# Kernel tuning notes

Measured on AMD Instinct MI355X. Metric: run time of the kernel, lower is better.

Reference implementation:

```python
import jax, jax.numpy as jnp
import numpy as np

B, T, F, U = 128, 512, 512, 256

def hard_sigmoid(x):
    # Keras K.hard_sigmoid
    return jnp.clip(0.2 * x + 0.5, 0.0, 1.0)

def setup_inputs() -> dict:
    key = jax.random.key(0)
    ks = jax.random.split(key, 10)
    def glorot(k, shp):
        fan_in, fan_out = shp[0], shp[-1]
        std = np.sqrt(2.0 / (fan_in + fan_out)).astype(np.float32)
        return jax.random.normal(k, shp, jnp.float32) * std
    return {
        "x": jax.random.normal(ks[0], (B, T, F), jnp.float32),
        "kernel": glorot(ks[1], (F, 4 * U)),
        "recurrent_kernel": glorot(ks[2], (U, 4 * U)),
        "attention_h": glorot(ks[3], (F + U, U)),
        "attention_c": glorot(ks[4], (F + U, U)),
        "attention1": glorot(ks[5], (2 * U + F, U)),
        "biase1": glorot(ks[6], (U,)),
        "attention2": glorot(ks[7], (U, 1)),
        "attention2_2": glorot(ks[8], (U, 1)),
        "biase2": glorot(ks[9], (U,)),
    }

def _run_direction(x_tbf, xg_tbg, rk, Wh, Wc, units):
    # x_tbf: (T,B,F); xg_tbg: (T,B,4U) precomputed x @ kernel (same math as per-step dot)
    Bn = x_tbf.shape[1]
    z = jnp.zeros((Bn, units), x_tbf.dtype)
    carry0 = (z, z, z, z, z, z, z, z)

    def att_weights(states, Ws, xt):
        # softmax over L2 norms of tanh(concat(state, x) @ W) for 4 history states
        scores = []
        for s, W in zip(states, Ws):
            a = jnp.tanh(jnp.concatenate([s, xt], axis=1) @ W)  # (B,U)
            scores.append(jnp.sqrt(jnp.sum(a * a, axis=1)))     # (B,)
        return jax.nn.softmax(jnp.stack(scores, axis=1), axis=1)  # (B,4)

    def step(carry, inp):
        xt, xg = inp
        h1, c1, h2, c2, h3, c3, h4, c4 = carry
        wh = att_weights([h1, h2, h3, h4], [Wh, Wh, Wh, Wh], xt)
        hmix = jax.nn.relu(wh[:, 0:1] * h1 + wh[:, 1:2] * h2 + wh[:, 2:3] * h3 + wh[:, 3:4] * h4)
        # NOTE: original code (faithfully kept) uses attention_h for the 4th cell-state score
        wc = att_weights([c1, c2, c3, c4], [Wc, Wc, Wc, Wh], xt)
        cmix = jax.nn.relu(wc[:, 0:1] * c1 + wc[:, 1:2] * c2 + wc[:, 2:3] * c3 + wc[:, 3:4] * c4)
        g = xg + hmix @ rk  # (B,4U), gate order [i, f, c, o]
        i = hard_sigmoid(g[:, :units])
        f = hard_sigmoid(g[:, units:2 * units])
        m = hard_sigmoid(g[:, 2 * units:3 * units])  # candidate uses hard_sigmoid in original
        o = hard_sigmoid(g[:, 3 * units:])
        c = f * cmix + i * m
        h = o * jnp.tanh(c)
        # history shift: [h, c, h_tm1, c_tm1, h_tm2, c_tm2, h_tm3, c_tm3]
        return (h, c, h1, c1, h2, c2, h3, c3), h

    _, hs = jax.lax.scan(step, carry0, (x_tbf, xg_tbg))
    return hs  # (T,B,U)

def reference(x, kernel, recurrent_kernel, attention_h, attention_c,
              attention1, biase1, attention2, attention2_2, biase2):
    units = recurrent_kernel.shape[0]
    x_tbf = jnp.transpose(x, (1, 0, 2))              # (T,B,F)
    xg = jnp.einsum('tbf,fg->tbg', x_tbf, kernel)    # (T,B,4U)
    fwd = _run_direction(x_tbf, xg, recurrent_kernel, attention_h, attention_c, units)
    bwd = _run_direction(x_tbf[::-1], xg[::-1], recurrent_kernel, attention_h, attention_c, units)[::-1]
    outs = jnp.concatenate([fwd, bwd], axis=-1)      # (T,B,2U)
    outs = jnp.transpose(outs, (1, 0, 2))            # (B,T,2U)
    # intra attention (vectorized over time, equivalent to the per-step loop + reshape)
    A11 = attention1[:2 * units, :]
    A12 = attention1[2 * units:, :]
    ha = jax.nn.relu(outs @ A11 + 0.0 * biase1) @ attention2        # (B,T,1)
    hb = jax.nn.relu(x @ A12 + 0.0 * biase2) @ attention2_2         # (B,T,1)
    return jnp.tanh(ha * outs + hb)                                  # (B,T,2U)
```

## Files before the change

kernel.cpp:

```cpp
#include <hip/hip_runtime.h>
#include <cstddef>
#include <cstdint>

#define DEVINL __device__ __forceinline__

constexpr int Bn = 128;
constexpr int Tn = 512;
constexpr int Fn = 512;
constexpr int Un = 256;
constexpr int Gn = 1024;
constexpr int RS = 5;

typedef _Float16 h2t   __attribute__((ext_vector_type(2)));
typedef _Float16 half4 __attribute__((ext_vector_type(4)));
typedef _Float16 half8 __attribute__((ext_vector_type(8)));
typedef float    f32x4 __attribute__((ext_vector_type(4)));

DEVINL float ftanh(float x) { float e = __expf(2.f * x); return 1.f - 2.f / (e + 1.f); }
DEVINL float hsig(float x)  { return fminf(fmaxf(fmaf(x, 0.2f, 0.5f), 0.f), 1.f); }

DEVINL void softmax4(float* s) {
    float mx = fmaxf(fmaxf(s[0], s[1]), fmaxf(s[2], s[3]));
    float e0 = __expf(s[0] - mx), e1 = __expf(s[1] - mx);
    float e2 = __expf(s[2] - mx), e3 = __expf(s[3] - mx);
    float inv = 1.f / (e0 + e1 + e2 + e3);
    s[0] = e0 * inv; s[1] = e1 * inv; s[2] = e2 * inv; s[3] = e3 * inv;
}

DEVINL float d2(unsigned int w, unsigned int h, float acc) {
#if __has_builtin(__builtin_amdgcn_fdot2)
    return __builtin_amdgcn_fdot2(__builtin_bit_cast(h2t, w), __builtin_bit_cast(h2t, h), acc, false);
#else
    h2t a = __builtin_bit_cast(h2t, w), b = __builtin_bit_cast(h2t, h);
    acc = fmaf((float)a.x, (float)b.x, acc);
    acc = fmaf((float)a.y, (float)b.y, acc);
    return acc;
#endif
}
DEVINL float dot8h(uint4 w, uint4 h, float acc) {
    acc = d2(w.x, h.x, acc);
    acc = d2(w.y, h.y, acc);
    acc = d2(w.z, h.z, acc);
    acc = d2(w.w, h.w, acc);
    return acc;
}

__global__ __launch_bounds__(256)
void pack_x(const float* __restrict__ x, _Float16* __restrict__ xh)
{
    size_t i = ((size_t)blockIdx.x * 256 + threadIdx.x) * 4;
    float4 v = *(const float4*)(x + i);
    half4 o;
    o.x = (_Float16)v.x; o.y = (_Float16)v.y; o.z = (_Float16)v.z; o.w = (_Float16)v.w;
    *(half4*)(xh + i) = o;
}

__global__ __launch_bounds__(256)
void wt_pack(const float* __restrict__ W, _Float16* __restrict__ Wt, int N)
{
    int total = N * 512;
    for (int e = blockIdx.x * 256 + threadIdx.x; e < total; e += gridDim.x * 256) {
        int n = e >> 9, k = e & 511;
        Wt[e] = (_Float16)W[(size_t)k * N + n];
    }
}

__global__ __launch_bounds__(256)
void pack_w(const float* __restrict__ rk, const float* __restrict__ ath,
            const float* __restrict__ atc,
            _Float16* __restrict__ rkP, _Float16* __restrict__ WhP,
            _Float16* __restrict__ WcP)
{
    int idx = blockIdx.x * 256 + threadIdx.x;
    const int stride = gridDim.x * 256;
    for (int e = idx; e < 32 * 1024 * 8; e += stride) {
        int i = e & 7, n = (e >> 3) & 1023, kc = e >> 13;
        rkP[e] = (_Float16)rk[(size_t)(kc * 8 + i) * Gn + n];
    }
    for (int e = idx; e < 32 * 256 * 8; e += stride) {
        int i = e & 7, n = (e >> 3) & 255, kc = e >> 11;
        WhP[e] = (_Float16)ath[(size_t)(kc * 8 + i) * Un + n];
        WcP[e] = (_Float16)atc[(size_t)(kc * 8 + i) * Un + n];
    }
}

template<bool TMAJ>
__global__ __launch_bounds__(256)
void gemm_mfma(const _Float16* __restrict__ A, const _Float16* __restrict__ Wt,
               int N, _Float16* __restrict__ out)
{
    __shared__ __align__(16) _Float16 As[64][40];
    __shared__ __align__(16) _Float16 Bs[64][40];
    const int tid = threadIdx.x;
    const int n0 = blockIdx.x * 64, m0 = blockIdx.y * 64;
    const int w = tid >> 6, lane = tid & 63;
    const int fr = lane & 15, quad = lane >> 4;
    const int srow = tid >> 2, sk = (tid & 3) * 8;

    f32x4 acc[4];
    #pragma unroll
    for (int i = 0; i < 4; i++) acc[i] = (f32x4){0.f, 0.f, 0.f, 0.f};

    const _Float16* ap = A  + (size_t)(m0 + srow) * 512 + sk;
    const _Float16* bp = Wt + (size_t)(n0 + srow) * 512 + sk;

    for (int k0 = 0; k0 < 512; k0 += 32) {
        uint4 av = *(const uint4*)(ap + k0);
        uint4 bv = *(const uint4*)(bp + k0);
        __syncthreads();
        *(uint4*)&As[srow][sk] = av;
        *(uint4*)&Bs[srow][sk] = bv;
        __syncthreads();
        half8 a = *(const half8*)&As[w * 16 + fr][quad * 8];
        #pragma unroll
        for (int nt = 0; nt < 4; nt++) {
            half8 b = *(const half8*)&Bs[nt * 16 + fr][quad * 8];
            acc[nt] = __builtin_amdgcn_mfma_f32_16x16x32_f16(a, b, acc[nt], 0, 0, 0);
        }
    }
    #pragma unroll
    for (int nt = 0; nt < 4; nt++) {
        int n = n0 + nt * 16 + fr;
        #pragma unroll
        for (int reg = 0; reg < 4; reg++) {
            int m = m0 + w * 16 + quad * 4 + reg;
            if (TMAJ) {
                int b = m >> 9, t = m & 511;
                out[((size_t)t * Bn + b) * N + n] = (_Float16)acc[nt][reg];
            } else {
                out[(size_t)m * N + n] = (_Float16)acc[nt][reg];
            }
        }
    }
}

__global__ __launch_bounds__(512)
void recurrence(const _Float16* __restrict__ xg,
                const _Float16* __restrict__ xWh,
                const _Float16* __restrict__ xWc,
                const _Float16* __restrict__ rkP,
                const _Float16* __restrict__ WhP,
                const _Float16* __restrict__ WcP,
                _Float16* __restrict__ outs)
{
    const int tid = threadIdx.x;
    const int d = blockIdx.x >> 7;
    const int b = blockIdx.x & 127;

    __shared__ float Hr[RS][Un], Cr[RS][Un];
    __shared__ float PHr[RS][Un], PCcr[RS][Un], PChr[RS][Un];
    __shared__ __align__(16) unsigned int hm_pk[128];
    __shared__ __align__(16) unsigned int Hpk[128], Cpk[128];
    __shared__ float gtmp[4][Un];
    __shared__ __align__(16) float red[8][4];

    for (int e = tid; e < RS * Un; e += 512) {
        ((float*)Hr)[e] = 0.f; ((float*)Cr)[e] = 0.f;
        ((float*)PHr)[e] = 0.f; ((float*)PCcr)[e] = 0.f; ((float*)PChr)[e] = 0.f;
    }
    __syncthreads();

    const int u = tid & 255;
    const int g = tid >> 8;
    const int lane = tid & 63;
    const int gwv = (tid >> 6) & 3;

    for (int t = 0; t < Tn; t++) {
        const int tt = d ? (Tn - 1 - t) : t;
        const int st = t % RS;
        int sj[4];
        #pragma unroll
        for (int j = 0; j < 4; j++) sj[j] = (t - 1 - j + 2 * RS) % RS;

        const size_t rowx = (size_t)tt * Bn + b;

        float xh = (float)xWh[rowx * Un + u];
        float xc = (float)xWc[rowx * Un + u];
        float xg0 = 0.f, xg1 = 0.f, xg2 = 0.f, xg3 = 0.f;
        if (tid < 256) {
            xg0 = (float)xg[rowx * Gn + u];
            xg1 = (float)xg[rowx * Gn + Un + u];
            xg2 = (float)xg[rowx * Gn + 2 * Un + u];
            xg3 = (float)xg[rowx * Gn + 3 * Un + u];
        }

        float vals[4];
        if (g == 0) {
            #pragma unroll
            for (int j = 0; j < 4; j++) {
                float ah = ftanh(PHr[sj[j]][u] + xh);
                vals[j] = ah * ah;
            }
        } else {
            #pragma unroll
            for (int j = 0; j < 4; j++) {
                float pc = (j < 3) ? PCcr[sj[j]][u] : PChr[sj[j]][u];
                float ac = ftanh(pc + ((j < 3) ? xc : xh));
                vals[j] = ac * ac;
            }
        }
        #pragma unroll
        for (int jj = 0; jj < 4; jj++) {
            float v = vals[jj];
            #pragma unroll
            for (int m = 32; m; m >>= 1) v += __shfl_xor(v, m, 64);
            if (lane == 0) red[g * 4 + jj][gwv] = v;
        }
        __syncthreads();

        float cmv = 0.f;
        if (tid < 256) {
            float sh[4], sc[4];
            #pragma unroll
            for (int j = 0; j < 4; j++) {
                float4 ph  = *(const float4*)red[j];
                float4 pcv = *(const float4*)red[4 + j];
                sh[j] = sqrtf(ph.x + ph.y + ph.z + ph.w);
                sc[j] = sqrtf(pcv.x + pcv.y + pcv.z + pcv.w);
            }
            softmax4(sh); softmax4(sc);
            float ha = 0.f, ca = 0.f;
            #pragma unroll
            for (int j = 0; j < 4; j++) {
                ha = fmaf(sh[j], Hr[sj[j]][u], ha);
                ca = fmaf(sc[j], Cr[sj[j]][u], ca);
            }
            float hmv = fmaxf(ha, 0.f);
            cmv = fmaxf(ca, 0.f);
            float ho = __shfl_xor(hmv, 1, 64);
            if (!(tid & 1)) {
                h2t pk; pk.x = (_Float16)hmv; pk.y = (_Float16)ho;
                hm_pk[u >> 1] = __builtin_bit_cast(unsigned int, pk);
            }
        }
        __syncthreads();

        {
            float a0 = 0.f, a1 = 0.f;
            const _Float16* p1 = rkP + (size_t)tid * 8;
            const _Float16* p2 = rkP + (size_t)(tid + 512) * 8;
            #pragma unroll 4
            for (int kc = 0; kc < 32; kc++) {
                uint4 w1 = *(const uint4*)(p1 + (size_t)kc * 8192);
                uint4 w2 = *(const uint4*)(p2 + (size_t)kc * 8192);
                uint4 h0 = *(const uint4*)&hm_pk[kc * 4];
                a0 = dot8h(w1, h0, a0);
                a1 = dot8h(w2, h0, a1);
            }
            int q = tid >> 8;
            gtmp[q][u] = a0;
            gtmp[q + 2][u] = a1;
        }
        __syncthreads();

        if (tid < 256) {
            float g0 = gtmp[0][u] + xg0;
            float g1 = gtmp[1][u] + xg1;
            float g2 = gtmp[2][u] + xg2;
            float g3 = gtmp[3][u] + xg3;
            float gi = hsig(g0), gf = hsig(g1), gm = hsig(g2), go = hsig(g3);
            float c = gf * cmv + gi * gm;
            float h = go * ftanh(c);
            Hr[st][u] = h;
            Cr[st][u] = c;
            outs[((size_t)b * Tn + tt) * 512 + d * 256 + u] = (_Float16)h;
            float hho = __shfl_xor(h, 1, 64);
            float cco = __shfl_xor(c, 1, 64);
            if (!(tid & 1)) {
                h2t pk1; pk1.x = (_Float16)h; pk1.y = (_Float16)hho;
                h2t pk2; pk2.x = (_Float16)c; pk2.y = (_Float16)cco;
                Hpk[u >> 1] = __builtin_bit_cast(unsigned int, pk1);
                Cpk[u >> 1] = __builtin_bit_cast(unsigned int, pk2);
            }
        }
        __syncthreads();

        if (tid < 256) {
            const int c = tid;
            const _Float16* pw = WhP + (size_t)c * 8;
            float ph = 0.f, pch = 0.f;
            #pragma unroll 4
            for (int kc = 0; kc < 32; kc++) {
                uint4 wv4 = *(const uint4*)(pw + (size_t)kc * 2048);
                uint4 Hv = *(const uint4*)&Hpk[kc * 4];
                uint4 Cv = *(const uint4*)&Cpk[kc * 4];
                ph  = dot8h(wv4, Hv, ph);
                pch = dot8h(wv4, Cv, pch);
            }
            PHr[st][c]  = ph;
            PChr[st][c] = pch;
        } else {
            const int c = tid - 256;
            const _Float16* pw = WcP + (size_t)c * 8;
            float pcc = 0.f;
            #pragma unroll 4
            for (int kc = 0; kc < 32; kc++) {
                uint4 wv4 = *(const uint4*)(pw + (size_t)kc * 2048);
                uint4 Cv = *(const uint4*)&Cpk[kc * 4];
                pcc = dot8h(wv4, Cv, pcc);
            }
            PCcr[st][c] = pcc;
        }
        __syncthreads();
    }
}

DEVINL void cvt8(uint4 v, float* f) {
    h2t p0 = __builtin_bit_cast(h2t, v.x), p1 = __builtin_bit_cast(h2t, v.y);
    h2t p2 = __builtin_bit_cast(h2t, v.z), p3 = __builtin_bit_cast(h2t, v.w);
    f[0] = (float)p0.x; f[1] = (float)p0.y; f[2] = (float)p1.x; f[3] = (float)p1.y;
    f[4] = (float)p2.x; f[5] = (float)p2.y; f[6] = (float)p3.x; f[7] = (float)p3.y;
}

__global__ __launch_bounds__(256)
void final2(const _Float16* __restrict__ t1, const _Float16* __restrict__ t2,
            const _Float16* __restrict__ outs16,
            const float* __restrict__ at2, const float* __restrict__ at22,
            float* __restrict__ out)
{
    __shared__ float has[8], hbs[8];
    const int tid = threadIdx.x;
    const size_t m0 = (size_t)blockIdx.x * 8;
    const int rr = tid >> 5, us = tid & 31;
    const size_t m = m0 + rr;

    uint4 v1 = *(const uint4*)(t1 + m * 256 + us * 8);
    uint4 v2 = *(const uint4*)(t2 + m * 256 + us * 8);
    float f1[8], f2[8];
    cvt8(v1, f1); cvt8(v2, f2);
    float4 wa0 = *(const float4*)(at2  + us * 8);
    float4 wa1 = *(const float4*)(at2  + us * 8 + 4);
    float4 wb0 = *(const float4*)(at22 + us * 8);
    float4 wb1 = *(const float4*)(at22 + us * 8 + 4);

    float pa = fmaxf(f1[0], 0.f) * wa0.x + fmaxf(f1[1], 0.f) * wa0.y
             + fmaxf(f1[2], 0.f) * wa0.z + fmaxf(f1[3], 0.f) * wa0.w
             + fmaxf(f1[4], 0.f) * wa1.x + fmaxf(f1[5], 0.f) * wa1.y
             + fmaxf(f1[6], 0.f) * wa1.z + fmaxf(f1[7], 0.f) * wa1.w;
    float pb = fmaxf(f2[0], 0.f) * wb0.x + fmaxf(f2[1], 0.f) * wb0.y
             + fmaxf(f2[2], 0.f) * wb0.z + fmaxf(f2[3], 0.f) * wb0.w
             + fmaxf(f2[4], 0.f) * wb1.x + fmaxf(f2[5], 0.f) * wb1.y
             + fmaxf(f2[6], 0.f) * wb1.z + fmaxf(f2[7], 0.f) * wb1.w;
    #pragma unroll
    for (int mm = 16; mm; mm >>= 1) {
        pa += __shfl_xor(pa, mm, 32);
        pb += __shfl_xor(pb, mm, 32);
    }
    if (us == 0) { has[rr] = pa; hbs[rr] = pb; }
    __syncthreads();

    for (int e = tid; e < 8 * 128; e += 256) {
        int r2 = e >> 7, k4 = (e & 127) * 4;
        size_t base = (m0 + r2) * 512 + k4;
        uint2 hv = *(const uint2*)(outs16 + base);
        h2t pA = __builtin_bit_cast(h2t, hv.x), pB = __builtin_bit_cast(h2t, hv.y);
        float hav = has[r2], hbv = hbs[r2];
        float4 o;
        o.x = ftanh(hav * (float)pA.x + hbv);
        o.y = ftanh(hav * (float)pA.y + hbv);
        o.z = ftanh(hav * (float)pB.x + hbv);
        o.w = ftanh(hav * (float)pB.y + hbv);
        *(float4*)(out + base) = o;
    }
}

extern "C" void kernel_launch(void* const* d_in, const int* in_sizes, int n_in,
                              void* d_out, int out_size, void* d_ws, size_t ws_size,
                              hipStream_t stream)
{
    (void)in_sizes; (void)n_in; (void)out_size; (void)ws_size;
    const float* x    = (const float*)d_in[0];
    const float* wk   = (const float*)d_in[1];
    const float* rk   = (const float*)d_in[2];
    const float* ath  = (const float*)d_in[3];
    const float* atc  = (const float*)d_in[4];
    const float* at1  = (const float*)d_in[5];
    const float* at2  = (const float*)d_in[7];
    const float* at22 = (const float*)d_in[8];
    float* out = (float*)d_out;

    char* p = (char*)d_ws;
    auto take = [&](size_t bytes) { char* q = p; p += (bytes + 255) & ~(size_t)255; return q; };
    _Float16* xg   = (_Float16*)take((size_t)Tn * Bn * Gn * 2);
    _Float16* xWh  = (_Float16*)take((size_t)Tn * Bn * Un * 2);
    _Float16* xWc  = (_Float16*)take((size_t)Tn * Bn * Un * 2);
    _Float16* A16  = (_Float16*)take((size_t)Bn * Tn * 512 * 2);
    _Float16* xf16 = (_Float16*)take((size_t)Bn * Tn * Fn * 2);
    _Float16* rkP  = (_Float16*)take((size_t)Un * Gn * 2);
    _Float16* WhP  = (_Float16*)take((size_t)Un * Un * 2);
    _Float16* WcP  = (_Float16*)take((size_t)Un * Un * 2);
    _Float16* Wt1  = (_Float16*)take((size_t)Gn * Fn * 2);
    _Float16* Wt2  = (_Float16*)take((size_t)Un * Fn * 2);
    _Float16* Wt3  = (_Float16*)take((size_t)Un * Fn * 2);
    _Float16* WtA  = (_Float16*)take((size_t)Un * Fn * 2);
    _Float16* WtB  = (_Float16*)take((size_t)Un * Fn * 2);
    _Float16* t1 = (_Float16*)xg;
    _Float16* t2 = t1 + (size_t)Bn * Tn * Un;

    pack_x<<<32768, 256, 0, stream>>>(x, xf16);
    wt_pack<<<2048, 256, 0, stream>>>(wk, Wt1, Gn);
    wt_pack<<<1024, 256, 0, stream>>>(ath + (size_t)Un * Un, Wt2, Un);
    wt_pack<<<1024, 256, 0, stream>>>(atc + (size_t)Un * Un, Wt3, Un);
    wt_pack<<<1024, 256, 0, stream>>>(at1, WtA, Un);
    wt_pack<<<1024, 256, 0, stream>>>(at1 + (size_t)512 * Un, WtB, Un);
    pack_w<<<64, 256, 0, stream>>>(rk, ath, atc, rkP, WhP, WcP);

    gemm_mfma<true><<<dim3(Gn / 64, (Bn * Tn) / 64), 256, 0, stream>>>(xf16, Wt1, Gn, xg);
    gemm_mfma<true><<<dim3(Un / 64, (Bn * Tn) / 64), 256, 0, stream>>>(xf16, Wt2, Un, xWh);
    gemm_mfma<true><<<dim3(Un / 64, (Bn * Tn) / 64), 256, 0, stream>>>(xf16, Wt3, Un, xWc);

    recurrence<<<dim3(256), dim3(512), 0, stream>>>(xg, xWh, xWc, rkP, WhP, WcP, A16);

    gemm_mfma<false><<<dim3(Un / 64, (Bn * Tn) / 64), 256, 0, stream>>>(A16,  WtA, Un, t1);
    gemm_mfma<false><<<dim3(Un / 64, (Bn * Tn) / 64), 256, 0, stream>>>(xf16, WtB, Un, t2);
    final2<<<(Bn * Tn) / 8, 256, 0, stream>>>(t1, t2, A16, at2, at22, out);
}
```

Baseline: 5.029 ms.

## Split recurrent weights across 8-block groups with global-memory barriers per step

Each group of 8 workgroups now handles 8 batch rows together, and each block keeps a 1/8 slice of the recurrent and attention weights resident in LDS (96KB dynamic shared memory). The block no longer streams the full weights from global or L2 every timestep. Intermediate vectors (hmix, h, c, the partial gate sums and the attention projections) are exchanged through global memory using relaxed atomics, with three to four counter-based inter-block barriers per timestep. This trades weight bandwidth for cross-block synchronization latency. It relies on all 256 blocks being co-resident, with a timeout guard to avoid deadlock.

Result: slower. 16.38 ms (+225.7%).

```diff
diff --git a/kernel.cpp b/kernel.cpp
--- a/kernel.cpp
+++ b/kernel.cpp
@@ -43,6 +43,19 @@
     acc = d2(w.z, h.z, acc);
     acc = d2(w.w, h.w, acc);
     return acc;
+}
+
+DEVINL void ast_u32(unsigned int* p, unsigned int v) {
+    __hip_atomic_store(p, v, __ATOMIC_RELAXED, __HIP_MEMORY_SCOPE_AGENT);
+}
+DEVINL unsigned int ald_u32(const unsigned int* p) {
+    return __hip_atomic_load(p, __ATOMIC_RELAXED, __HIP_MEMORY_SCOPE_AGENT);
+}
+DEVINL void ast_f32(float* p, float v) {
+    __hip_atomic_store(p, v, __ATOMIC_RELAXED, __HIP_MEMORY_SCOPE_AGENT);
+}
+DEVINL float ald_f32(const float* p) {
+    return __hip_atomic_load(p, __ATOMIC_RELAXED, __HIP_MEMORY_SCOPE_AGENT);
 }
 
 __global__ __launch_bounds__(256)
@@ -141,29 +154,79 @@
                 const _Float16* __restrict__ rkP,
                 const _Float16* __restrict__ WhP,
                 const _Float16* __restrict__ WcP,
-                _Float16* __restrict__ outs)
+                _Float16* __restrict__ outs,
+                unsigned int* __restrict__ Xhm,
+                unsigned int* __restrict__ XH,
+                unsigned int* __restrict__ XC,
+                float* __restrict__ Xg,
+                float* __restrict__ Xph,
+                float* __restrict__ Xpch,
+                float* __restrict__ Xpcc,
+                unsigned int* __restrict__ cnt)
 {
     const int tid = threadIdx.x;
-    const int d = blockIdx.x >> 7;
-    const int b = blockIdx.x & 127;
+    const int grp = blockIdx.x & 31;
+    const int s   = blockIdx.x >> 5;
+    const int rowId = grp * 8 + s;
+    const int d = rowId >> 7, b = rowId & 127;
 
     __shared__ float Hr[RS][Un], Cr[RS][Un];
     __shared__ float PHr[RS][Un], PCcr[RS][Un], PChr[RS][Un];
-    __shared__ __align__(16) unsigned int hm_pk[128];
-    __shared__ __align__(16) unsigned int Hpk[128], Cpk[128];
     __shared__ float gtmp[4][Un];
+    __shared__ __align__(16) unsigned int hmS[8][128];
+    __shared__ __align__(16) unsigned int HSs[8][128], CSs[8][128];
     __shared__ __align__(16) float red[8][4];
-
+    __shared__ int sync_dead;
+
+    extern __shared__ uint4 dynv[];
+    uint4* rkA = dynv;
+    uint4* WhA = dynv + 32 * 128;
+    uint4* WcA = WhA + 32 * 32;
+
+    {
+        const uint4* rkG = (const uint4*)rkP;
+        for (int e = tid; e < 32 * 128; e += 512) {
+            int kc = e >> 7, c = e & 127;
+            rkA[e] = rkG[kc * 1024 + s * 128 + c];
+        }
+        const uint4* whG = (const uint4*)WhP;
+        const uint4* wcG = (const uint4*)WcP;
+        for (int e = tid; e < 32 * 32; e += 512) {
+            int kc = e >> 5, c = e & 31;
+            WhA[e] = whG[kc * 256 + s * 32 + c];
+            WcA[e] = wcG[kc * 256 + s * 32 + c];
+        }
+    }
     for (int e = tid; e < RS * Un; e += 512) {
         ((float*)Hr)[e] = 0.f; ((float*)Cr)[e] = 0.f;
         ((float*)PHr)[e] = 0.f; ((float*)PCcr)[e] = 0.f; ((float*)PChr)[e] = 0.f;
     }
+    if (tid == 0) sync_dead = 0;
     __syncthreads();
+
+    unsigned int* myCnt = cnt + grp * 64;
+    unsigned int tgt = 8;
 
     const int u = tid & 255;
     const int g = tid >> 8;
     const int lane = tid & 63;
     const int gwv = (tid >> 6) & 3;
+    const size_t gb128 = (size_t)grp * 8 * 128;
+
+    auto gsync = [&](unsigned int target) {
+        __syncthreads();
+        if (tid == 0) {
+            __hip_atomic_fetch_add(myCnt, 1u, __ATOMIC_ACQ_REL, __HIP_MEMORY_SCOPE_AGENT);
+            if (!sync_dead) {
+                int guard = 0;
+                while (__hip_atomic_load(myCnt, __ATOMIC_ACQUIRE, __HIP_MEMORY_SCOPE_AGENT) < target) {
+                    __builtin_amdgcn_s_sleep(2);
+                    if (++guard > 2000000) { sync_dead = 1; break; }
+                }
+            }
+        }
+        __syncthreads();
+    };
 
     for (int t = 0; t < Tn; t++) {
         const int tt = d ? (Tn - 1 - t) : t;
@@ -171,7 +234,6 @@
         int sj[4];
         #pragma unroll
         for (int j = 0; j < 4; j++) sj[j] = (t - 1 - j + 2 * RS) % RS;
-
         const size_t rowx = (size_t)tt * Bn + b;
 
         float xh = (float)xWh[rowx * Un + u];
@@ -182,6 +244,18 @@
             xg1 = (float)xg[rowx * Gn + Un + u];
             xg2 = (float)xg[rowx * Gn + 2 * Un + u];
             xg3 = (float)xg[rowx * Gn + 3 * Un + u];
+        }
+
+        if (t > 0) {
+            if (tid < 256) {
+                int slot = (t - 1) % RS;
+                int src = tid >> 5, c5 = tid & 31;
+                size_t pb = ((size_t)(grp * 8 + src) * 8 + s) * 32 + c5;
+                PHr[slot][tid]  = ald_f32(Xph + pb);
+                PChr[slot][tid] = ald_f32(Xpch + pb);
+                PCcr[slot][tid] = ald_f32(Xpcc + pb);
+            }
+            __syncthreads();
         }
 
         float vals[4];
@@ -230,29 +304,38 @@
             float ho = __shfl_xor(hmv, 1, 64);
             if (!(tid & 1)) {
                 h2t pk; pk.x = (_Float16)hmv; pk.y = (_Float16)ho;
-                hm_pk[u >> 1] = __builtin_bit_cast(unsigned int, pk);
-            }
-        }
-        __syncthreads();
-
+                ast_u32(Xhm + (size_t)rowId * 128 + (u >> 1),
+                        __builtin_bit_cast(unsigned int, pk));
+            }
+        }
+        gsync(tgt); tgt += 8;
+
+        for (int e = tid; e < 1024; e += 512)
+            hmS[e >> 7][e & 127] = ald_u32(Xhm + gb128 + e);
+        __syncthreads();
         {
+            const int col = tid & 127, rp = tid >> 7;
+            const uint4* hv0 = (const uint4*)hmS[rp * 2];
+            const uint4* hv1 = (const uint4*)hmS[rp * 2 + 1];
             float a0 = 0.f, a1 = 0.f;
-            const _Float16* p1 = rkP + (size_t)tid * 8;
-            const _Float16* p2 = rkP + (size_t)(tid + 512) * 8;
             #pragma unroll 4
             for (int kc = 0; kc < 32; kc++) {
-                uint4 w1 = *(const uint4*)(p1 + (size_t)kc * 8192);
-                uint4 w2 = *(const uint4*)(p2 + (size_t)kc * 8192);
-                uint4 h0 = *(const uint4*)&hm_pk[kc * 4];
-                a0 = dot8h(w1, h0, a0);
-                a1 = dot8h(w2, h0, a1);
-            }
-            int q = tid >> 8;
-            gtmp[q][u] = a0;
-            gtmp[q + 2][u] = a1;
-        }
-        __syncthreads();
-
+                uint4 w = rkA[kc * 128 + col];
+                a0 = dot8h(w, hv0[kc], a0);
+                a1 = dot8h(w, hv1[kc], a1);
+            }
+            ast_f32(Xg + ((size_t)rowId * 8 + rp * 2) * 128 + col, a0);
+            ast_f32(Xg + ((size_t)rowId * 8 + rp * 2 + 1) * 128 + col, a1);
+        }
+        gsync(tgt); tgt += 8;
+
+        for (int e = tid; e < 1024; e += 512) {
+            int src = e >> 7, cl = e & 127;
+            float gv = ald_f32(Xg + ((size_t)(grp * 8 + src) * 8 + s) * 128 + cl);
+            int C = src * 128 + cl;
+            gtmp[C >> 8][C & 255] = gv;
+        }
+        __syncthreads();
         if (tid < 256) {
             float g0 = gtmp[0][u] + xg0;
             float g1 = gtmp[1][u] + xg1;
@@ -269,39 +352,45 @@
             if (!(tid & 1)) {
                 h2t pk1; pk1.x = (_Float16)h; pk1.y = (_Float16)hho;
                 h2t pk2; pk2.x = (_Float16)c; pk2.y = (_Float16)cco;
-                Hpk[u >> 1] = __builtin_bit_cast(unsigned int, pk1);
-                Cpk[u >> 1] = __builtin_bit_cast(unsigned int, pk2);
-            }
-        }
-        __syncthreads();
-
+                ast_u32(XH + (size_t)rowId * 128 + (u >> 1),
+                        __builtin_bit_cast(unsigned int, pk1));
+                ast_u32(XC + (size_t)rowId * 128 + (u >> 1),
+                        __builtin_bit_cast(unsigned int, pk2));
+            }
+        }
+        gsync(tgt); tgt += 8;
+
+        for (int e = tid; e < 1024; e += 512) {
+            HSs[e >> 7][e & 127] = ald_u32(XH + gb128 + e);
+            CSs[e >> 7][e & 127] = ald_u32(XC + gb128 + e);
+        }
+        __syncthreads();
         if (tid < 256) {
-            const int c = tid;
-            const _Float16* pw = WhP + (size_t)c * 8;
+            int rr = tid >> 5, c = tid & 31;
+            const uint4* Hv = (const uint4*)HSs[rr];
+            const uint4* Cv = (const uint4*)CSs[rr];
             float ph = 0.f, pch = 0.f;
             #pragma unroll 4
             for (int kc = 0; kc < 32; kc++) {
-                uint4 wv4 = *(const uint4*)(pw + (size_t)kc * 2048);
-                uint4 Hv = *(const uint4*)&Hpk[kc * 4];
-                uint4 Cv = *(const uint4*)&Cpk[kc * 4];
-                ph  = dot8h(wv4, Hv, ph);
-                pch = dot8h(wv4, Cv, pch);
-            }
-            PHr[st][c]  = ph;
-            PChr[st][c] = pch;
+                uint4 w = WhA[kc * 32 + c];
+                ph  = dot8h(w, Hv[kc], ph);
+                pch = dot8h(w, Cv[kc], pch);
+            }
+            size_t pb = ((size_t)rowId * 8 + rr) * 32 + c;
+            ast_f32(Xph + pb, ph);
+            ast_f32(Xpch + pb, pch);
         } else {
-            const int c = tid - 256;
-            const _Float16* pw = WcP + (size_t)c * 8;
+            int i = tid - 256, rr = i >> 5, c = i & 31;
+            const uint4* Cv = (const uint4*)CSs[rr];
             float pcc = 0.f;
             #pragma unroll 4
             for (int kc = 0; kc < 32; kc++) {
-                uint4 wv4 = *(const uint4*)(pw + (size_t)kc * 2048);
-                uint4 Cv = *(const uint4*)&Cpk[kc * 4];
-                pcc = dot8h(wv4, Cv, pcc);
-            }
-            PCcr[st][c] = pcc;
-        }
-        __syncthreads();
+                uint4 w = WcA[kc * 32 + c];
+                pcc = dot8h(w, Cv[kc], pcc);
+            }
+            ast_f32(Xpcc + ((size_t)rowId * 8 + rr) * 32 + c, pcc);
+        }
+        gsync(tgt); tgt += 8;
     }
 }
 
@@ -394,6 +483,14 @@
     _Float16* Wt3  = (_Float16*)take((size_t)Un * Fn * 2);
     _Float16* WtA  = (_Float16*)take((size_t)Un * Fn * 2);
     _Float16* WtB  = (_Float16*)take((size_t)Un * Fn * 2);
+    unsigned int* Xhm = (unsigned int*)take(32 * 8 * 128 * 4);
+    unsigned int* XH  = (unsigned int*)take(32 * 8 * 128 * 4);
+    unsigned int* XC  = (unsigned int*)take(32 * 8 * 128 * 4);
+    float* Xg   = (float*)take((size_t)32 * 8 * 8 * 128 * 4);
+    float* Xph  = (float*)take(32 * 8 * 8 * 32 * 4);
+    float* Xpch = (float*)take(32 * 8 * 8 * 32 * 4);
+    float* Xpcc = (float*)take(32 * 8 * 8 * 32 * 4);
+    unsigned int* cnt = (unsigned int*)take(32 * 64 * 4);
     _Float16* t1 = (_Float16*)xg;
     _Float16* t2 = t1 + (size_t)Bn * Tn * Un;
 
@@ -409,7 +506,12 @@
     gemm_mfma<true><<<dim3(Un / 64, (Bn * Tn) / 64), 256, 0, stream>>>(xf16, Wt2, Un, xWh);
     gemm_mfma<true><<<dim3(Un / 64, (Bn * Tn) / 64), 256, 0, stream>>>(xf16, Wt3, Un, xWc);
 
-    recurrence<<<dim3(256), dim3(512), 0, stream>>>(xg, xWh, xWc, rkP, WhP, WcP, A16);
+    hipMemsetAsync(cnt, 0, 32 * 64 * 4, stream);
+    hipFuncSetAttribute(reinterpret_cast<const void*>(recurrence),
+                        hipFuncAttributeMaxDynamicSharedMemorySize, 98304);
+    recurrence<<<dim3(256), dim3(512), 98304, stream>>>(
+        xg, xWh, xWc, rkP, WhP, WcP, A16,
+        Xhm, XH, XC, Xg, Xph, Xpch, Xpcc, cnt);
 
     gemm_mfma<false><<<dim3(Un / 64, (Bn * Tn) / 64), 256, 0, stream>>>(A16,  WtA, Un, t1);
     gemm_mfma<false><<<dim3(Un / 64, (Bn * Tn) / 64), 256, 0, stream>>>(xf16, WtB, Un, t2);
```
